# Kernel optimization log

Hardware: AMD Instinct MI355X
Metric: run time of the kernel (lower is better)

## Reference

```python
import jax, jax.numpy as jnp
import numpy as np

N_NODES = 50000
N_EDGES = 800000
IN_DIM, H1, H2, OUT_DIM = 128, 117, 42, 24


def _glorot(key, fan_in, fan_out):
    lim = (6.0 / (fan_in + fan_out)) ** 0.5
    return jax.random.uniform(key, (fan_in, fan_out), jnp.float32, -lim, lim)


def setup_inputs() -> dict:
    key = jax.random.key(0)
    ks = jax.random.split(key, 16)
    x = jax.random.normal(ks[0], (N_NODES, IN_DIM), jnp.float32)
    edge_index = jax.random.randint(ks[1], (2, N_EDGES), 0, N_NODES, dtype=jnp.int64)
    dims = [(IN_DIM, H1), (H1, H2), (H2, OUT_DIM), (H2, OUT_DIM)]
    names = ["1", "2", "mu", "lv"]
    inp = {"x": x, "edge_index": edge_index}
    for i, ((di, do), nm) in enumerate(zip(dims, names)):
        inp[f"Wl_{nm}"] = _glorot(ks[2 + 3 * i], di, do)      # weight on aggregated neighbors
        inp[f"Wr_{nm}"] = _glorot(ks[3 + 3 * i], di, do)      # root (self) weight
        inp[f"b_{nm}"] = jnp.zeros((do,), jnp.float32)
    return inp


def _sage_conv(x, src, dst, Wl, Wr, b):
    # mean-aggregate source features onto target nodes (PyG SAGEConv, aggr='mean')
    agg = jax.ops.segment_sum(x[src], dst, num_segments=N_NODES)      # [N, d_in]
    deg = jax.ops.segment_sum(jnp.ones((src.shape[0], 1), x.dtype), dst,
                              num_segments=N_NODES)                    # [N, 1]
    agg = agg / jnp.maximum(deg, 1.0)
    return agg @ Wl + x @ Wr + b


def reference(x, edge_index, Wl_1, Wr_1, b_1, Wl_2, Wr_2, b_2,
              Wl_mu, Wr_mu, b_mu, Wl_lv, Wr_lv, b_lv):
    src, dst = edge_index[0], edge_index[1]
    h = jax.nn.relu(_sage_conv(x, src, dst, Wl_1, Wr_1, b_1))          # dropout = identity (eval)
    h = jax.nn.relu(_sage_conv(h, src, dst, Wl_2, Wr_2, b_2))
    mu = _sage_conv(h, src, dst, Wl_mu, Wr_mu, b_mu)
    logvar = _sage_conv(h, src, dst, Wl_lv, Wr_lv, b_lv)
    return (mu, logvar)
```

## Files before the change

kernel.cpp:

```cpp
#include <hip/hip_runtime.h>

#define N_NODES 50000
#define N_EDGES 800000
#define CAP 64
#define ZROW 50000
#define BSTRIDE 96

typedef _Float16 f16;
typedef unsigned short u16;
typedef f16 f16x2 __attribute__((ext_vector_type(2)));
typedef f16 f16x4 __attribute__((ext_vector_type(4)));
typedef f16 f16x8 __attribute__((ext_vector_type(8)));
typedef float f32x4 __attribute__((ext_vector_type(4)));

#if __has_builtin(__builtin_amdgcn_fdot2)
#define FDOT2(a, b, c) __builtin_amdgcn_fdot2((a), (b), (c), false)
#else
#define FDOT2(a, b, c) ((c) + (float)(a).x * (float)(b).x + (float)(a).y * (float)(b).y)
#endif

__global__ void k_fillpack(u16* __restrict__ bucket,
                           f16* __restrict__ t1l, f16* __restrict__ t2l,
                           f16* __restrict__ p,
                           const float* __restrict__ Wl1, const float* __restrict__ Wr1,
                           const float* __restrict__ Wl2, const float* __restrict__ Wr2,
                           const float* __restrict__ Wlm, const float* __restrict__ Wrm,
                           const float* __restrict__ Wlv, const float* __restrict__ Wrv,
                           f16* __restrict__ w1b, f16* __restrict__ w2b,
                           f16* __restrict__ w3b) {
    int gt = blockIdx.x * 256 + threadIdx.x;
    if (gt < N_NODES * 12) {
        int c = gt % 12;
        uint4 val = {0xC350C350u, 0xC350C350u, 0xC350C350u, 0xC350C350u};
        if (c == 0) val.x = 0u;
        ((uint4*)bucket)[gt] = val;
    }
    if (blockIdx.x == 2343) {
        int t = threadIdx.x;
        if (t < 64)       ((unsigned*)t1l)[(size_t)ZROW * 64 + t] = 0u;
        else if (t < 96)  ((unsigned*)t2l)[(size_t)ZROW * 32 + (t - 64)] = 0u;
        else if (t < 128) ((unsigned*)p)[(size_t)ZROW * 32 + (t - 96)] = 0u;
    }
    if (gt < 15 * 4 * 64 * 8) {
        int f = gt >> 9, r = gt & 511;
        int lane = r >> 3, j = r & 7;
        int nt = f >> 2, s = f & 3;
        int k = s * 32 + (lane >> 4) * 8 + j;
        int col = nt * 16 + (lane & 15);
        float v = 0.f;
        if (col < 117) v = Wl1[k * 117 + col];
        else if (col < 234) v = Wr1[k * 117 + (col - 117)];
        w1b[gt] = (f16)v;
    }
    if (gt < 6 * 4 * 64 * 8) {
        int f = gt >> 9, r = gt & 511;
        int lane = r >> 3, j = r & 7;
        int nt = f >> 2, s = f & 3;
        int k = s * 32 + (lane >> 4) * 8 + j;
        int col = nt * 16 + (lane & 15);
        float v = 0.f;
        if (k < 117) {
            if (col < 42)                     v = Wl2[k * 42 + col];
            else if (col >= 48 && col < 90)   v = Wr2[k * 42 + (col - 48)];
        }
        w2b[gt] = (f16)v;
    }
    if (gt < 6 * 2 * 64 * 8) {
        int f = gt >> 9, r = gt & 511;
        int lane = r >> 3, j = r & 7;
        int ct = f >> 1, s = f & 1;
        int k = s * 32 + (lane >> 4) * 8 + j;
        int col = ct * 16 + (lane & 15);
        float v = 0.f;
        if (k < 42) {
            if (col < 24)      v = Wlm[k * 24 + col];
            else if (col < 48) v = Wlv[k * 24 + (col - 24)];
            else if (col < 72) v = Wrm[k * 24 + (col - 48)];
            else               v = Wrv[k * 24 + (col - 72)];
        }
        w3b[gt] = (f16)v;
    }
}

__global__ __launch_bounds__(256) void k_bg(const int* __restrict__ ei,
                        u16* __restrict__ bucket,
                        const float* __restrict__ x,
                        const f16* __restrict__ w1b, const float* __restrict__ b1,
                        f16* __restrict__ t1l, float* __restrict__ t1r) {
    int t = threadIdx.x;
    int e = blockIdx.x * 256 + t;
    int se = ei[e];
    int de = ei[N_EDGES + e];
    int pos = atomicAdd((int*)(bucket + (size_t)de * BSTRIDE), 1);

    int base = blockIdx.x * 16;
    __shared__ __align__(16) f16 xa[16 * 128];
    {
        int row = t >> 4, kc = t & 15;
        const float4* xp = (const float4*)(x + (size_t)(base + row) * 128 + kc * 8);
        float4 x0 = xp[0], x1 = xp[1];
        f16x8 hv;
        hv[0] = (f16)x0.x; hv[1] = (f16)x0.y; hv[2] = (f16)x0.z; hv[3] = (f16)x0.w;
        hv[4] = (f16)x1.x; hv[5] = (f16)x1.y; hv[6] = (f16)x1.z; hv[7] = (f16)x1.w;
        int byte = row * 256 + ((kc ^ (row & 7)) << 4);
        *(f16x8*)((char*)xa + byte) = hv;
    }
    __syncthreads();
    int lane = t & 63, w = t >> 6;
    int hi = lane >> 4, lo = lane & 15;
    f16x8 a[4];
#pragma unroll
    for (int s = 0; s < 4; ++s) {
        int kchunk = s * 4 + hi;
        int byte = lo * 256 + ((kchunk ^ (lo & 7)) << 4);
        a[s] = *(const f16x8*)((const char*)xa + byte);
    }
    int ntiles = (w < 3) ? 4 : 3;
    for (int i = 0; i < ntiles; ++i) {
        int nt = w * 4 + i;
        const f16x8* bp = (const f16x8*)w1b + (size_t)(nt * 4) * 64 + lane;
        f32x4 acc = {0.f, 0.f, 0.f, 0.f};
#pragma unroll
        for (int s = 0; s < 4; ++s)
            acc = __builtin_amdgcn_mfma_f32_16x16x32_f16(a[s], bp[s * 64], acc, 0, 0, 0);
        int gcol = nt * 16 + lo;
#pragma unroll
        for (int r = 0; r < 4; ++r) {
            int grow = base + hi * 4 + r;
            float val = acc[r];
            if (gcol < 117) {
                t1l[(size_t)grow * 128 + gcol] = (f16)val;
            } else if (nt == 7) {
                t1l[(size_t)grow * 128 + gcol] = (f16)0.f;
            }
            if (gcol >= 117) {
                int c2 = gcol - 117;
                if (c2 < 117)      t1r[(size_t)grow * 120 + c2] = val + b1[c2];
                else if (c2 < 120) t1r[(size_t)grow * 120 + c2] = 0.f;
            }
        }
    }
    if (pos < CAP) bucket[(size_t)de * BSTRIDE + 8 + pos] = (u16)se;
}

__global__ __launch_bounds__(512) void k_fused1(
        const f16* __restrict__ t1l, const float* __restrict__ t1r,
        const u16* __restrict__ bucket,
        const f16* __restrict__ w2b, const float* __restrict__ b2,
        f16* __restrict__ t2l, float* __restrict__ s2) {
    __shared__ __align__(16) f16 h1[32 * 128];
    __shared__ __align__(16) u16 ids[32 * 72];
    __shared__ int cnts[32];
    int t = threadIdx.x;
    int lane = t & 63, w = t >> 6;
    int tilebase = blockIdx.x * 32;
    if (t < 288) {
        int row = t / 9, c = t % 9;
        uint4 q = *(const uint4*)(bucket + (size_t)(tilebase + row) * BSTRIDE + c * 8);
        if (c == 0) cnts[row] = (int)q.x;
        else *(uint4*)(ids + row * 72 + (c - 1) * 8) = q;
    }
    __syncthreads();
    int g = (lane < 60) ? (lane / 15) : 3;
    int d = (lane < 60) ? (lane - g * 15) : 14;
    int nl = w * 4 + g;
    int i_my = tilebase + nl;
    int c = (i_my < N_NODES && lane < 60) ? cnts[nl] : 0;
    int n = min(c, CAP);
    float deg = fmaxf((float)c, 1.f);
    int n0 = __builtin_amdgcn_readlane(n, 0),  n1 = __builtin_amdgcn_readlane(n, 15);
    int n2 = __builtin_amdgcn_readlane(n, 30), n3 = __builtin_amdgcn_readlane(n, 45);
    int nmax = max(max(n0, n1), max(n2, n3));
    float acc[8] = {0.f, 0.f, 0.f, 0.f, 0.f, 0.f, 0.f, 0.f};
    const char* tb = (const char*)t1l;
    unsigned doff = (unsigned)d * 16;
    const f16x2 e10 = {(f16)1.f, (f16)0.f};
    const f16x2 e01 = {(f16)0.f, (f16)1.f};
    int idb = nl * 72;
    for (int e0 = 0; e0 < nmax; e0 += 8) {
        f16x8 v[8];
#pragma unroll
        for (int u = 0; u < 8; ++u) {
            unsigned id = ids[idb + e0 + u];
            v[u] = *(const f16x8*)(tb + id * 256u + doff);
        }
#pragma unroll
        for (int u = 0; u < 8; ++u) {
            const f16x2* pv = (const f16x2*)&v[u];
#pragma unroll
            for (int j = 0; j < 4; ++j) {
                acc[2 * j]     = FDOT2(pv[j], e10, acc[2 * j]);
                acc[2 * j + 1] = FDOT2(pv[j], e01, acc[2 * j + 1]);
            }
        }
    }
    if (lane < 60) {
        int i_ld = (i_my < N_NODES) ? i_my : 0;
        const float4* sp = (const float4*)(t1r + (size_t)i_ld * 120 + 8 * d);
        float4 s0 = sp[0], s1 = sp[1];
        float sv[8] = {s0.x, s0.y, s0.z, s0.w, s1.x, s1.y, s1.z, s1.w};
        f16x8 hv;
#pragma unroll
        for (int j = 0; j < 8; ++j) hv[j] = (f16)fmaxf(acc[j] / deg + sv[j], 0.f);
        int byte = nl * 256 + ((d ^ (nl & 7)) << 4);
        *(f16x8*)((char*)h1 + byte) = hv;
    } else {
        int row = w * 4 + (lane - 60);
        int byte = row * 256 + ((15 ^ (row & 7)) << 4);
        f16x8 z = {};
        *(f16x8*)((char*)h1 + byte) = z;
    }
    __syncthreads();
    int lo = lane & 15, hi = lane >> 4;
    for (int jj = w; jj < 12; jj += 8) {
        int ct = jj >> 1, rh = jj & 1;
        int row = rh * 16 + lo;
        f16x8 a[4];
#pragma unroll
        for (int s = 0; s < 4; ++s) {
            int kc = s * 4 + hi;
            a[s] = *(const f16x8*)((const char*)h1 + row * 256 + ((kc ^ (row & 7)) << 4));
        }
        const f16x8* bp = (const f16x8*)w2b + (size_t)(ct * 4) * 64 + lane;
        f32x4 acc4 = {0.f, 0.f, 0.f, 0.f};
#pragma unroll
        for (int s = 0; s < 4; ++s)
            acc4 = __builtin_amdgcn_mfma_f32_16x16x32_f16(a[s], bp[s * 64], acc4, 0, 0, 0);
        int col = ct * 16 + lo;
#pragma unroll
        for (int r = 0; r < 4; ++r) {
            int node = tilebase + rh * 16 + hi * 4 + r;
            if (node < N_NODES) {
                if (col < 48)      t2l[(size_t)node * 64 + col] = (f16)acc4[r];
                else if (col < 90) s2[(size_t)node * 42 + (col - 48)] = acc4[r] + b2[col - 48];
            }
        }
    }
}

__global__ __launch_bounds__(128) void k_fused2(
        const f16* __restrict__ t2l, const float* __restrict__ s2,
        const u16* __restrict__ bucket,
        const f16* __restrict__ w3b,
        const float* __restrict__ bm, const float* __restrict__ bv,
        f16* __restrict__ p, float* __restrict__ out) {
    __shared__ __align__(16) f16 h2[16 * 64];
    __shared__ __align__(16) u16 ids[16 * 72];
    __shared__ int cnts[16];
    int t = threadIdx.x;
    int lane = t & 63, wv = t >> 6;
    int nb = blockIdx.x * 16;
    for (int s = t; s < 144; s += 128) {
        int row = s / 9, c = s % 9;
        uint4 q = *(const uint4*)(bucket + (size_t)(nb + row) * BSTRIDE + c * 8);
        if (c == 0) cnts[row] = (int)q.x;
        else *(uint4*)(ids + row * 72 + (c - 1) * 8) = q;
    }
    __syncthreads();
    int g = (lane < 48) ? (lane / 6) : 7;
    int d = (lane < 48) ? (lane - g * 6) : 5;
    int nl = wv * 8 + g;
    int i_my = nb + nl;
    int c = (lane < 48) ? cnts[nl] : 0;
    int n = min(c, CAP);
    float deg = fmaxf((float)c, 1.f);
    int nmax = n;
#pragma unroll
    for (int m = 1; m < 64; m <<= 1) nmax = max(nmax, __shfl_xor(nmax, m));
    float acc[8] = {0.f, 0.f, 0.f, 0.f, 0.f, 0.f, 0.f, 0.f};
    const char* tb = (const char*)t2l;
    unsigned doff = (unsigned)d * 16;
    const f16x2 e10 = {(f16)1.f, (f16)0.f};
    const f16x2 e01 = {(f16)0.f, (f16)1.f};
    int idb = nl * 72;
    for (int e0 = 0; e0 < nmax; e0 += 8) {
        f16x8 v[8];
#pragma unroll
        for (int u = 0; u < 8; ++u) {
            unsigned id = ids[idb + e0 + u];
            v[u] = *(const f16x8*)(tb + id * 128u + doff);
        }
#pragma unroll
        for (int u = 0; u < 8; ++u) {
            const f16x2* pv = (const f16x2*)&v[u];
#pragma unroll
            for (int j = 0; j < 4; ++j) {
                acc[2 * j]     = FDOT2(pv[j], e10, acc[2 * j]);
                acc[2 * j + 1] = FDOT2(pv[j], e01, acc[2 * j + 1]);
            }
        }
    }
    if (lane < 48) {
        float sv[8];
        if (d < 5) {
            const float4* sp = (const float4*)(s2 + (size_t)i_my * 42 + 8 * d);
            float4 s0 = sp[0], s1 = sp[1];
            sv[0] = s0.x; sv[1] = s0.y; sv[2] = s0.z; sv[3] = s0.w;
            sv[4] = s1.x; sv[5] = s1.y; sv[6] = s1.z; sv[7] = s1.w;
        } else {
            float2 s0 = *(const float2*)(s2 + (size_t)i_my * 42 + 40);
            sv[0] = s0.x; sv[1] = s0.y;
            sv[2] = sv[3] = sv[4] = sv[5] = sv[6] = sv[7] = 0.f;
        }
        f16x8 hv;
#pragma unroll
        for (int j = 0; j < 8; ++j) hv[j] = (f16)fmaxf(acc[j] / deg + sv[j], 0.f);
        int byte = nl * 128 + ((d ^ (nl & 7)) << 4);
        *(f16x8*)((char*)h2 + byte) = hv;
    } else {
        int j = lane - 48;
        int row = wv * 8 + (j >> 1);
        int chunk = 6 + (j & 1);
        int byte = row * 128 + ((chunk ^ (row & 7)) << 4);
        f16x8 z = {};
        *(f16x8*)((char*)h2 + byte) = z;
    }
    __syncthreads();
    int lo = lane & 15, hi = lane >> 4;
    f16x8 a2[2];
#pragma unroll
    for (int s = 0; s < 2; ++s) {
        int kc = s * 4 + hi;
        a2[s] = *(const f16x8*)((const char*)h2 + lo * 128 + ((kc ^ (lo & 7)) << 4));
    }
#pragma unroll
    for (int i = 0; i < 3; ++i) {
        int ct = wv * 3 + i;
        const f16x8* bp = (const f16x8*)w3b + (size_t)(ct * 2) * 64 + lane;
        f32x4 acc4 = {0.f, 0.f, 0.f, 0.f};
        acc4 = __builtin_amdgcn_mfma_f32_16x16x32_f16(a2[0], bp[0], acc4, 0, 0, 0);
        acc4 = __builtin_amdgcn_mfma_f32_16x16x32_f16(a2[1], bp[64], acc4, 0, 0, 0);
        int col = ct * 16 + lo;
#pragma unroll
        for (int r = 0; r < 4; ++r) {
            int node = nb + hi * 4 + r;
            if (col < 48) {
                p[(size_t)node * 64 + col] = (f16)acc4[r];
            } else {
                int o = col - 48;
                if (o < 24) out[(size_t)node * 24 + o] = acc4[r] + bm[o];
                else out[(size_t)N_NODES * 24 + (size_t)node * 24 + (o - 24)] = acc4[r] + bv[o - 24];
            }
        }
    }
}

__global__ __launch_bounds__(128) void k_final(
        const f16* __restrict__ p, const u16* __restrict__ bucket,
        float* __restrict__ out) {
    __shared__ __align__(16) u16 ids[20 * 72];
    __shared__ int cnts[20];
    int t = threadIdx.x;
    int lane = t & 63, wv = t >> 6;
    int nb = blockIdx.x * 20;
    for (int s = t; s < 180; s += 128) {
        int row = s / 9, c = s % 9;
        uint4 q = *(const uint4*)(bucket + (size_t)(nb + row) * BSTRIDE + c * 8);
        if (c == 0) cnts[row] = (int)q.x;
        else *(uint4*)(ids + row * 72 + (c - 1) * 8) = q;
    }
    __syncthreads();
    int g = (lane < 60) ? (lane / 6) : 9;
    int d = (lane < 60) ? (lane - g * 6) : 5;
    int nl = wv * 10 + g;
    int i_my = nb + nl;
    int c = (lane < 60) ? cnts[nl] : 0;
    int n = min(c, CAP);
    float deg = fmaxf((float)c, 1.f);
    int nmax = n;
#pragma unroll
    for (int m = 1; m < 64; m <<= 1) nmax = max(nmax, __shfl_xor(nmax, m));
    float acc[8] = {0.f, 0.f, 0.f, 0.f, 0.f, 0.f, 0.f, 0.f};
    const char* pb = (const char*)p;
    unsigned doff = (unsigned)d * 16;
    const f16x2 e10 = {(f16)1.f, (f16)0.f};
    const f16x2 e01 = {(f16)0.f, (f16)1.f};
    int idb = nl * 72;
    for (int e0 = 0; e0 < nmax; e0 += 8) {
        f16x8 v[8];
#pragma unroll
        for (int u = 0; u < 8; ++u) {
            unsigned id = ids[idb + e0 + u];
            v[u] = *(const f16x8*)(pb + id * 128u + doff);
        }
#pragma unroll
        for (int u = 0; u < 8; ++u) {
            const f16x2* pv = (const f16x2*)&v[u];
#pragma unroll
            for (int j = 0; j < 4; ++j) {
                acc[2 * j]     = FDOT2(pv[j], e10, acc[2 * j]);
                acc[2 * j + 1] = FDOT2(pv[j], e01, acc[2 * j + 1]);
            }
        }
    }
    if (lane < 60) {
        float rdeg = 1.f / deg;
        size_t base = (d < 3) ? ((size_t)i_my * 24 + 8 * d)
                              : ((size_t)N_NODES * 24 + (size_t)i_my * 24 + 8 * (d - 3));
        float4 o0 = *(const float4*)(out + base);
        float4 o1 = *(const float4*)(out + base + 4);
        o0.x += acc[0] * rdeg; o0.y += acc[1] * rdeg;
        o0.z += acc[2] * rdeg; o0.w += acc[3] * rdeg;
        o1.x += acc[4] * rdeg; o1.y += acc[5] * rdeg;
        o1.z += acc[6] * rdeg; o1.w += acc[7] * rdeg;
        *(float4*)(out + base) = o0;
        *(float4*)(out + base + 4) = o1;
    }
}

extern "C" void kernel_launch(void* const* d_in, const int* in_sizes, int n_in,
                              void* d_out, int out_size, void* d_ws, size_t ws_size,
                              hipStream_t stream) {
    const float* x   = (const float*)d_in[0];
    const int*   ei  = (const int*)d_in[1];
    const float* Wl1 = (const float*)d_in[2];
    const float* Wr1 = (const float*)d_in[3];
    const float* b1  = (const float*)d_in[4];
    const float* Wl2 = (const float*)d_in[5];
    const float* Wr2 = (const float*)d_in[6];
    const float* b2  = (const float*)d_in[7];
    const float* Wlm = (const float*)d_in[8];
    const float* Wrm = (const float*)d_in[9];
    const float* bm  = (const float*)d_in[10];
    const float* Wlv = (const float*)d_in[11];
    const float* Wrv = (const float*)d_in[12];
    const float* bv  = (const float*)d_in[13];
    float* out = (float*)d_out;

    char* ws = (char*)d_ws;
    u16*   bucket = (u16*)(ws);
    f16*   t1l    = (f16*)(ws + 9600000);
    float* t1r    = (float*)(ws + 22400256);
    f16*   t2l    = (f16*)(ws + 46400256);
    float* s2     = (float*)(ws + 52800384);
    f16*   w1b    = (f16*)(ws + 52800384);
    f16*   p      = (f16*)(ws + 61200384);
    f16*   w2b    = (f16*)(ws + 67600512);
    f16*   w3b    = (f16*)(ws + 67625088);

    k_fillpack<<<2344, 256, 0, stream>>>(bucket, t1l, t2l, p,
                                         Wl1, Wr1, Wl2, Wr2, Wlm, Wrm, Wlv, Wrv,
                                         w1b, w2b, w3b);
    k_bg<<<3125, 256, 0, stream>>>(ei, bucket, x, w1b, b1, t1l, t1r);
    k_fused1<<<1563, 512, 0, stream>>>(t1l, t1r, bucket, w2b, b2, t2l, s2);
    k_fused2<<<3125, 128, 0, stream>>>(t2l, s2, bucket, w3b, bm, bv, p, out);
    k_final<<<2500, 128, 0, stream>>>(p, bucket, out);
}
```

Measured before the change: 210.1 us.

## Aggregate h2 before projecting in final layer instead of transforming then aggregating

The final SAGE layer now stores the 42-wide h2 activations (48-padded fp16 rows of 96 bytes) and gathers and mean-aggregates those. It then applies the neighbor weights with MFMA in k_final, replacing the old path that projected first to a 48-wide p (128-byte rows) and aggregated p. The gather moves fewer bytes per edge, at the cost of an extra matmul and LDS staging in the final kernel, and of fewer nodes per block there (16 instead of 20). The bucket fill also switches to a nontemporal store.

After: 224.0 us. 1.07x slower.

```diff
diff --git a/kernel.cpp b/kernel.cpp
--- a/kernel.cpp
+++ b/kernel.cpp
@@ -21,7 +21,7 @@
 
 __global__ void k_fillpack(u16* __restrict__ bucket,
                            f16* __restrict__ t1l, f16* __restrict__ t2l,
-                           f16* __restrict__ p,
+                           f16* __restrict__ h2g,
                            const float* __restrict__ Wl1, const float* __restrict__ Wr1,
                            const float* __restrict__ Wl2, const float* __restrict__ Wr2,
                            const float* __restrict__ Wlm, const float* __restrict__ Wrm,
@@ -39,7 +39,7 @@
         int t = threadIdx.x;
         if (t < 64)       ((unsigned*)t1l)[(size_t)ZROW * 64 + t] = 0u;
         else if (t < 96)  ((unsigned*)t2l)[(size_t)ZROW * 32 + (t - 64)] = 0u;
-        else if (t < 128) ((unsigned*)p)[(size_t)ZROW * 32 + (t - 96)] = 0u;
+        else if (t < 120) ((unsigned*)h2g)[(size_t)ZROW * 24 + (t - 96)] = 0u;
     }
     if (gt < 15 * 4 * 64 * 8) {
         int f = gt >> 9, r = gt & 511;
@@ -140,7 +140,8 @@
             }
         }
     }
-    if (pos < CAP) bucket[(size_t)de * BSTRIDE + 8 + pos] = (u16)se;
+    if (pos < CAP)
+        __builtin_nontemporal_store((u16)se, bucket + (size_t)de * BSTRIDE + 8 + pos);
 }
 
 __global__ __launch_bounds__(512) void k_fused1(
@@ -243,7 +244,7 @@
         const u16* __restrict__ bucket,
         const f16* __restrict__ w3b,
         const float* __restrict__ bm, const float* __restrict__ bv,
-        f16* __restrict__ p, float* __restrict__ out) {
+        f16* __restrict__ h2g, float* __restrict__ out) {
     __shared__ __align__(16) f16 h2[16 * 64];
     __shared__ __align__(16) u16 ids[16 * 72];
     __shared__ int cnts[16];
@@ -307,6 +308,7 @@
         for (int j = 0; j < 8; ++j) hv[j] = (f16)fmaxf(acc[j] / deg + sv[j], 0.f);
         int byte = nl * 128 + ((d ^ (nl & 7)) << 4);
         *(f16x8*)((char*)h2 + byte) = hv;
+        *(f16x8*)(h2g + (size_t)i_my * 48 + d * 8) = hv;
     } else {
         int j = lane - 48;
         int row = wv * 8 + (j >> 1);
@@ -323,55 +325,48 @@
         int kc = s * 4 + hi;
         a2[s] = *(const f16x8*)((const char*)h2 + lo * 128 + ((kc ^ (lo & 7)) << 4));
     }
-#pragma unroll
-    for (int i = 0; i < 3; ++i) {
-        int ct = wv * 3 + i;
+    for (int ct = 3 + wv; ct < 6; ct += 2) {
         const f16x8* bp = (const f16x8*)w3b + (size_t)(ct * 2) * 64 + lane;
         f32x4 acc4 = {0.f, 0.f, 0.f, 0.f};
         acc4 = __builtin_amdgcn_mfma_f32_16x16x32_f16(a2[0], bp[0], acc4, 0, 0, 0);
         acc4 = __builtin_amdgcn_mfma_f32_16x16x32_f16(a2[1], bp[64], acc4, 0, 0, 0);
-        int col = ct * 16 + lo;
+        int o = ct * 16 + lo - 48;
 #pragma unroll
         for (int r = 0; r < 4; ++r) {
             int node = nb + hi * 4 + r;
-            if (col < 48) {
-                p[(size_t)node * 64 + col] = (f16)acc4[r];
-            } else {
-                int o = col - 48;
-                if (o < 24) out[(size_t)node * 24 + o] = acc4[r] + bm[o];
-                else out[(size_t)N_NODES * 24 + (size_t)node * 24 + (o - 24)] = acc4[r] + bv[o - 24];
-            }
+            if (o < 24) out[(size_t)node * 24 + o] = acc4[r] + bm[o];
+            else out[(size_t)N_NODES * 24 + (size_t)node * 24 + (o - 24)] = acc4[r] + bv[o - 24];
         }
     }
 }
 
 __global__ __launch_bounds__(128) void k_final(
-        const f16* __restrict__ p, const u16* __restrict__ bucket,
-        float* __restrict__ out) {
-    __shared__ __align__(16) u16 ids[20 * 72];
-    __shared__ int cnts[20];
+        const f16* __restrict__ h2g, const u16* __restrict__ bucket,
+        const f16* __restrict__ w3b, float* __restrict__ out) {
+    __shared__ __align__(16) f16 hh[16 * 64];
+    __shared__ __align__(16) u16 ids[16 * 72];
+    __shared__ int cnts[16];
     int t = threadIdx.x;
     int lane = t & 63, wv = t >> 6;
-    int nb = blockIdx.x * 20;
-    for (int s = t; s < 180; s += 128) {
+    int nb = blockIdx.x * 16;
+    for (int s = t; s < 144; s += 128) {
         int row = s / 9, c = s % 9;
         uint4 q = *(const uint4*)(bucket + (size_t)(nb + row) * BSTRIDE + c * 8);
         if (c == 0) cnts[row] = (int)q.x;
         else *(uint4*)(ids + row * 72 + (c - 1) * 8) = q;
     }
     __syncthreads();
-    int g = (lane < 60) ? (lane / 6) : 9;
-    int d = (lane < 60) ? (lane - g * 6) : 5;
-    int nl = wv * 10 + g;
-    int i_my = nb + nl;
-    int c = (lane < 60) ? cnts[nl] : 0;
+    int g = (lane < 48) ? (lane / 6) : 7;
+    int d = (lane < 48) ? (lane - g * 6) : 5;
+    int nl = wv * 8 + g;
+    int c = (lane < 48) ? cnts[nl] : 0;
     int n = min(c, CAP);
     float deg = fmaxf((float)c, 1.f);
     int nmax = n;
 #pragma unroll
     for (int m = 1; m < 64; m <<= 1) nmax = max(nmax, __shfl_xor(nmax, m));
     float acc[8] = {0.f, 0.f, 0.f, 0.f, 0.f, 0.f, 0.f, 0.f};
-    const char* pb = (const char*)p;
+    const char* hb = (const char*)h2g;
     unsigned doff = (unsigned)d * 16;
     const f16x2 e10 = {(f16)1.f, (f16)0.f};
     const f16x2 e01 = {(f16)0.f, (f16)1.f};
@@ -381,7 +376,7 @@
 #pragma unroll
         for (int u = 0; u < 8; ++u) {
             unsigned id = ids[idb + e0 + u];
-            v[u] = *(const f16x8*)(pb + id * 128u + doff);
+            v[u] = *(const f16x8*)(hb + id * 96u + doff);
         }
 #pragma unroll
         for (int u = 0; u < 8; ++u) {
@@ -393,18 +388,42 @@
             }
         }
     }
-    if (lane < 60) {
+    if (lane < 48) {
         float rdeg = 1.f / deg;
-        size_t base = (d < 3) ? ((size_t)i_my * 24 + 8 * d)
-                              : ((size_t)N_NODES * 24 + (size_t)i_my * 24 + 8 * (d - 3));
-        float4 o0 = *(const float4*)(out + base);
-        float4 o1 = *(const float4*)(out + base + 4);
-        o0.x += acc[0] * rdeg; o0.y += acc[1] * rdeg;
-        o0.z += acc[2] * rdeg; o0.w += acc[3] * rdeg;
-        o1.x += acc[4] * rdeg; o1.y += acc[5] * rdeg;
-        o1.z += acc[6] * rdeg; o1.w += acc[7] * rdeg;
-        *(float4*)(out + base) = o0;
-        *(float4*)(out + base + 4) = o1;
+        f16x8 hv;
+#pragma unroll
+        for (int j = 0; j < 8; ++j) hv[j] = (f16)(acc[j] * rdeg);
+        int byte = nl * 128 + ((d ^ (nl & 7)) << 4);
+        *(f16x8*)((char*)hh + byte) = hv;
+    } else {
+        int j = lane - 48;
+        int row = wv * 8 + (j >> 1);
+        int chunk = 6 + (j & 1);
+        int byte = row * 128 + ((chunk ^ (row & 7)) << 4);
+        f16x8 z = {};
+        *(f16x8*)((char*)hh + byte) = z;
+    }
+    __syncthreads();
+    int lo = lane & 15, hi = lane >> 4;
+    f16x8 a2[2];
+#pragma unroll
+    for (int s = 0; s < 2; ++s) {
+        int kc = s * 4 + hi;
+        a2[s] = *(const f16x8*)((const char*)hh + lo * 128 + ((kc ^ (lo & 7)) << 4));
+    }
+    for (int ct = wv; ct < 3; ct += 2) {
+        const f16x8* bp = (const f16x8*)w3b + (size_t)(ct * 2) * 64 + lane;
+        f32x4 acc4 = {0.f, 0.f, 0.f, 0.f};
+        acc4 = __builtin_amdgcn_mfma_f32_16x16x32_f16(a2[0], bp[0], acc4, 0, 0, 0);
+        acc4 = __builtin_amdgcn_mfma_f32_16x16x32_f16(a2[1], bp[64], acc4, 0, 0, 0);
+        int o = ct * 16 + lo;
+#pragma unroll
+        for (int r = 0; r < 4; ++r) {
+            int node = nb + hi * 4 + r;
+            size_t addr = (o < 24) ? ((size_t)node * 24 + o)
+                                   : ((size_t)N_NODES * 24 + (size_t)node * 24 + (o - 24));
+            out[addr] += acc4[r];
+        }
     }
 }
 
@@ -434,15 +453,15 @@
     f16*   t2l    = (f16*)(ws + 46400256);
     float* s2     = (float*)(ws + 52800384);
     f16*   w1b    = (f16*)(ws + 52800384);
-    f16*   p      = (f16*)(ws + 61200384);
-    f16*   w2b    = (f16*)(ws + 67600512);
-    f16*   w3b    = (f16*)(ws + 67625088);
-
-    k_fillpack<<<2344, 256, 0, stream>>>(bucket, t1l, t2l, p,
+    f16*   h2g    = (f16*)(ws + 61200384);
+    f16*   w2b    = (f16*)(ws + 66000512);
+    f16*   w3b    = (f16*)(ws + 66025088);
+
+    k_fillpack<<<2344, 256, 0, stream>>>(bucket, t1l, t2l, h2g,
                                          Wl1, Wr1, Wl2, Wr2, Wlm, Wrm, Wlv, Wrv,
                                          w1b, w2b, w3b);
     k_bg<<<3125, 256, 0, stream>>>(ei, bucket, x, w1b, b1, t1l, t1r);
     k_fused1<<<1563, 512, 0, stream>>>(t1l, t1r, bucket, w2b, b2, t2l, s2);
-    k_fused2<<<3125, 128, 0, stream>>>(t2l, s2, bucket, w3b, bm, bv, p, out);
-    k_final<<<2500, 128, 0, stream>>>(p, bucket, out);
-}
+    k_fused2<<<3125, 128, 0, stream>>>(t2l, s2, bucket, w3b, bm, bv, h2g, out);
+    k_final<<<3125, 128, 0, stream>>>(h2g, bucket, w3b, out);
+}
```

## Split layer-1 gather and layer-2 GEMM into separate kernels with column slicing

Applied to the files above, without the earlier changes.

Replaces the fused layer-1 aggregation plus MFMA kernel with two kernels. The first gathers neighbors with 16-node blocks split into four column slices, four edges processed in parallel per node with shuffle reduction, and writes h1 to global memory. The second loads h1 tiles and runs the MFMA projection. The intent is more parallelism and less per-node serialization in the gather. The cost is an extra global round-trip for h1 and one more launch. The p zero-row init moves into k_fused2 and the workspace is relaid out so h1 aliases p.

New measurement: 236.0 us. 12.3% more time.

```diff
diff --git a/kernel.cpp b/kernel.cpp
--- a/kernel.cpp
+++ b/kernel.cpp
@@ -21,7 +21,6 @@
 
 __global__ void k_fillpack(u16* __restrict__ bucket,
                            f16* __restrict__ t1l, f16* __restrict__ t2l,
-                           f16* __restrict__ p,
                            const float* __restrict__ Wl1, const float* __restrict__ Wr1,
                            const float* __restrict__ Wl2, const float* __restrict__ Wr2,
                            const float* __restrict__ Wlm, const float* __restrict__ Wrm,
@@ -39,7 +38,6 @@
         int t = threadIdx.x;
         if (t < 64)       ((unsigned*)t1l)[(size_t)ZROW * 64 + t] = 0u;
         else if (t < 96)  ((unsigned*)t2l)[(size_t)ZROW * 32 + (t - 64)] = 0u;
-        else if (t < 128) ((unsigned*)p)[(size_t)ZROW * 32 + (t - 96)] = 0u;
     }
     if (gt < 15 * 4 * 64 * 8) {
         int f = gt >> 9, r = gt & 511;
@@ -143,84 +141,94 @@
     if (pos < CAP) bucket[(size_t)de * BSTRIDE + 8 + pos] = (u16)se;
 }
 
-__global__ __launch_bounds__(512) void k_fused1(
+__global__ __launch_bounds__(256) void k_f1a(
         const f16* __restrict__ t1l, const float* __restrict__ t1r,
-        const u16* __restrict__ bucket,
-        const f16* __restrict__ w2b, const float* __restrict__ b2,
-        f16* __restrict__ t2l, float* __restrict__ s2) {
-    __shared__ __align__(16) f16 h1[32 * 128];
-    __shared__ __align__(16) u16 ids[32 * 72];
-    __shared__ int cnts[32];
+        const u16* __restrict__ bucket, f16* __restrict__ h1) {
+    __shared__ __align__(16) u16 ids[16 * 72];
+    __shared__ int cnts[16];
     int t = threadIdx.x;
     int lane = t & 63, w = t >> 6;
-    int tilebase = blockIdx.x * 32;
-    if (t < 288) {
+    int bid = blockIdx.x;
+    int slice = bid & 3;
+    int nb = (bid >> 2) * 16;
+    if (t < 144) {
         int row = t / 9, c = t % 9;
-        uint4 q = *(const uint4*)(bucket + (size_t)(tilebase + row) * BSTRIDE + c * 8);
+        uint4 q = *(const uint4*)(bucket + (size_t)(nb + row) * BSTRIDE + c * 8);
         if (c == 0) cnts[row] = (int)q.x;
         else *(uint4*)(ids + row * 72 + (c - 1) * 8) = q;
     }
     __syncthreads();
-    int g = (lane < 60) ? (lane / 15) : 3;
-    int d = (lane < 60) ? (lane - g * 15) : 14;
-    int nl = w * 4 + g;
-    int i_my = tilebase + nl;
-    int c = (i_my < N_NODES && lane < 60) ? cnts[nl] : 0;
+    int nl = w * 4 + (lane >> 4);
+    int gl = lane & 15;
+    int epos = gl >> 2;
+    int chunk = gl & 3;
+    int i_my = nb + nl;
+    int c = cnts[nl];
     int n = min(c, CAP);
     float deg = fmaxf((float)c, 1.f);
-    int n0 = __builtin_amdgcn_readlane(n, 0),  n1 = __builtin_amdgcn_readlane(n, 15);
-    int n2 = __builtin_amdgcn_readlane(n, 30), n3 = __builtin_amdgcn_readlane(n, 45);
-    int nmax = max(max(n0, n1), max(n2, n3));
     float acc[8] = {0.f, 0.f, 0.f, 0.f, 0.f, 0.f, 0.f, 0.f};
     const char* tb = (const char*)t1l;
-    unsigned doff = (unsigned)d * 16;
+    unsigned soff = (unsigned)slice * 64 + (unsigned)chunk * 16;
     const f16x2 e10 = {(f16)1.f, (f16)0.f};
     const f16x2 e01 = {(f16)0.f, (f16)1.f};
     int idb = nl * 72;
-    for (int e0 = 0; e0 < nmax; e0 += 8) {
-        f16x8 v[8];
-#pragma unroll
-        for (int u = 0; u < 8; ++u) {
-            unsigned id = ids[idb + e0 + u];
-            v[u] = *(const f16x8*)(tb + id * 256u + doff);
-        }
-#pragma unroll
-        for (int u = 0; u < 8; ++u) {
-            const f16x2* pv = (const f16x2*)&v[u];
-#pragma unroll
-            for (int j = 0; j < 4; ++j) {
-                acc[2 * j]     = FDOT2(pv[j], e10, acc[2 * j]);
-                acc[2 * j + 1] = FDOT2(pv[j], e01, acc[2 * j + 1]);
-            }
-        }
-    }
-    if (lane < 60) {
-        int i_ld = (i_my < N_NODES) ? i_my : 0;
-        const float4* sp = (const float4*)(t1r + (size_t)i_ld * 120 + 8 * d);
-        float4 s0 = sp[0], s1 = sp[1];
-        float sv[8] = {s0.x, s0.y, s0.z, s0.w, s1.x, s1.y, s1.z, s1.w};
+    for (int e0 = 0; e0 < n; e0 += 4) {
+        unsigned id = ids[idb + e0 + epos];
+        f16x8 v = *(const f16x8*)(tb + id * 256u + soff);
+        const f16x2* pv = (const f16x2*)&v;
+#pragma unroll
+        for (int j = 0; j < 4; ++j) {
+            acc[2 * j]     = FDOT2(pv[j], e10, acc[2 * j]);
+            acc[2 * j + 1] = FDOT2(pv[j], e01, acc[2 * j + 1]);
+        }
+    }
+#pragma unroll
+    for (int j = 0; j < 8; ++j) {
+        acc[j] += __shfl_xor(acc[j], 4);
+        acc[j] += __shfl_xor(acc[j], 8);
+    }
+    if (epos == 0) {
+        int colbase = slice * 32 + chunk * 8;
         f16x8 hv;
-#pragma unroll
-        for (int j = 0; j < 8; ++j) hv[j] = (f16)fmaxf(acc[j] / deg + sv[j], 0.f);
-        int byte = nl * 256 + ((d ^ (nl & 7)) << 4);
-        *(f16x8*)((char*)h1 + byte) = hv;
-    } else {
-        int row = w * 4 + (lane - 60);
-        int byte = row * 256 + ((15 ^ (row & 7)) << 4);
-        f16x8 z = {};
-        *(f16x8*)((char*)h1 + byte) = z;
-    }
-    __syncthreads();
-    int lo = lane & 15, hi = lane >> 4;
-    for (int jj = w; jj < 12; jj += 8) {
-        int ct = jj >> 1, rh = jj & 1;
-        int row = rh * 16 + lo;
-        f16x8 a[4];
-#pragma unroll
-        for (int s = 0; s < 4; ++s) {
-            int kc = s * 4 + hi;
-            a[s] = *(const f16x8*)((const char*)h1 + row * 256 + ((kc ^ (row & 7)) << 4));
-        }
+        if (colbase >= 120) {
+            f16x8 z = {};
+            hv = z;
+        } else {
+            const float* sp = t1r + (size_t)i_my * 120 + colbase;
+            float4 s0 = *(const float4*)sp;
+            float4 s1 = *(const float4*)(sp + 4);
+            float sv[8] = {s0.x, s0.y, s0.z, s0.w, s1.x, s1.y, s1.z, s1.w};
+#pragma unroll
+            for (int j = 0; j < 8; ++j) hv[j] = (f16)fmaxf(acc[j] / deg + sv[j], 0.f);
+        }
+        *(f16x8*)(h1 + (size_t)i_my * 128 + colbase) = hv;
+    }
+}
+
+__global__ __launch_bounds__(256) void k_f1b(
+        const f16* __restrict__ h1, const f16* __restrict__ w2b,
+        const float* __restrict__ b2,
+        f16* __restrict__ t2l, float* __restrict__ s2) {
+    int base = blockIdx.x * 16;
+    int t = threadIdx.x;
+    __shared__ __align__(16) f16 ha[16 * 128];
+    {
+        int row = t >> 4, kc = t & 15;
+        f16x8 hv = *(const f16x8*)(h1 + (size_t)(base + row) * 128 + kc * 8);
+        int byte = row * 256 + ((kc ^ (row & 7)) << 4);
+        *(f16x8*)((char*)ha + byte) = hv;
+    }
+    __syncthreads();
+    int lane = t & 63, w = t >> 6;
+    int hi = lane >> 4, lo = lane & 15;
+    f16x8 a[4];
+#pragma unroll
+    for (int s = 0; s < 4; ++s) {
+        int kc = s * 4 + hi;
+        int byte = lo * 256 + ((kc ^ (lo & 7)) << 4);
+        a[s] = *(const f16x8*)((const char*)ha + byte);
+    }
+    for (int ct = w; ct < 6; ct += 4) {
         const f16x8* bp = (const f16x8*)w2b + (size_t)(ct * 4) * 64 + lane;
         f32x4 acc4 = {0.f, 0.f, 0.f, 0.f};
 #pragma unroll
@@ -229,11 +237,9 @@
         int col = ct * 16 + lo;
 #pragma unroll
         for (int r = 0; r < 4; ++r) {
-            int node = tilebase + rh * 16 + hi * 4 + r;
-            if (node < N_NODES) {
-                if (col < 48)      t2l[(size_t)node * 64 + col] = (f16)acc4[r];
-                else if (col < 90) s2[(size_t)node * 42 + (col - 48)] = acc4[r] + b2[col - 48];
-            }
+            int node = base + hi * 4 + r;
+            if (col < 48)      t2l[(size_t)node * 64 + col] = (f16)acc4[r];
+            else if (col < 90) s2[(size_t)node * 42 + (col - 48)] = acc4[r] + b2[col - 48];
         }
     }
 }
@@ -250,6 +256,8 @@
     int t = threadIdx.x;
     int lane = t & 63, wv = t >> 6;
     int nb = blockIdx.x * 16;
+    if (blockIdx.x == 0 && t < 32)
+        ((unsigned*)p)[(size_t)ZROW * 32 + t] = 0u;
     for (int s = t; s < 144; s += 128) {
         int row = s / 9, c = s % 9;
         uint4 q = *(const uint4*)(bucket + (size_t)(nb + row) * BSTRIDE + c * 8);
@@ -428,21 +436,23 @@
     float* out = (float*)d_out;
 
     char* ws = (char*)d_ws;
-    u16*   bucket = (u16*)(ws);
-    f16*   t1l    = (f16*)(ws + 9600000);
-    float* t1r    = (float*)(ws + 22400256);
-    f16*   t2l    = (f16*)(ws + 46400256);
-    float* s2     = (float*)(ws + 52800384);
-    f16*   w1b    = (f16*)(ws + 52800384);
-    f16*   p      = (f16*)(ws + 61200384);
-    f16*   w2b    = (f16*)(ws + 67600512);
-    f16*   w3b    = (f16*)(ws + 67625088);
-
-    k_fillpack<<<2344, 256, 0, stream>>>(bucket, t1l, t2l, p,
+    f16*   w2b    = (f16*)(ws);
+    f16*   w3b    = (f16*)(ws + 24576);
+    u16*   bucket = (u16*)(ws + 40960);
+    f16*   t1l    = (f16*)(ws + 9640960);
+    float* t1r    = (float*)(ws + 22441216);
+    f16*   t2l    = (f16*)(ws + 46441216);
+    float* s2     = (float*)(ws + 52841344);
+    f16*   w1b    = (f16*)(ws + 52841344);
+    f16*   h1     = (f16*)(ws + 61241344);
+    f16*   p      = (f16*)(ws + 61241344);
+
+    k_fillpack<<<2344, 256, 0, stream>>>(bucket, t1l, t2l,
                                          Wl1, Wr1, Wl2, Wr2, Wlm, Wrm, Wlv, Wrv,
                                          w1b, w2b, w3b);
     k_bg<<<3125, 256, 0, stream>>>(ei, bucket, x, w1b, b1, t1l, t1r);
-    k_fused1<<<1563, 512, 0, stream>>>(t1l, t1r, bucket, w2b, b2, t2l, s2);
+    k_f1a<<<12500, 256, 0, stream>>>(t1l, t1r, bucket, h1);
+    k_f1b<<<3125, 256, 0, stream>>>(h1, w2b, b2, t2l, s2);
     k_fused2<<<3125, 128, 0, stream>>>(t2l, s2, bucket, w3b, bm, bv, p, out);
     k_final<<<2500, 128, 0, stream>>>(p, bucket, out);
 }
```
